# Performance work log

Measured on AMD Instinct MI355X. Metric: run time of the kernel, lower is better.

## Reference

```python
import jax, jax.numpy as jnp
import numpy as np

B, NG, H, G, T0, T1 = 4096, 3000, 6, 30, 500, 50  # batch, genes, hidden, genes/term, leaf terms, mid terms
EPS = 1e-5  # BatchNorm1d default eps


def _bn(x, gamma, beta):
    # training-mode BatchNorm1d: biased batch stats over the batch axis
    m = x.mean(axis=0)
    v = ((x - m) ** 2).mean(axis=0)
    return gamma * (x - m) / jnp.sqrt(v + EPS) + beta


def setup_inputs() -> dict:
    key = jax.random.key(0)
    ks = iter(jax.random.split(key, 32))
    rn = lambda shape, s=0.05: jax.random.normal(next(ks), shape, dtype=jnp.float32) * s
    return dict(
        cell_features=jax.random.normal(next(ks), (B, NG), dtype=jnp.float32),
        Wdg=rn((T0 + T1 + 1, G, NG)), bdg=rn((T0 + T1 + 1, G)),
        W0=rn((T0, H, G)), b0=rn((T0, H)), gam0=jnp.ones((T0, H), jnp.float32), bet0=jnp.zeros((T0, H), jnp.float32),
        aw0=rn((T0, H)), ab0=rn((T0,)), av0=rn((T0,)), ac0=rn((T0,)),
        W1=rn((T1, H, 10 * H + G)), b1=rn((T1, H)), gam1=jnp.ones((T1, H), jnp.float32), bet1=jnp.zeros((T1, H), jnp.float32),
        aw1=rn((T1, H)), ab1=rn((T1,)), av1=rn((T1,)), ac1=rn((T1,)),
        W2=rn((H, T1 * H + G)), b2=rn((H,)), gam2=jnp.ones((H,), jnp.float32), bet2=jnp.zeros((H,), jnp.float32),
        aw2=rn((H,)), ab2=rn(()), av2=rn(()), ac2=rn(()),
    )


def reference(cell_features, Wdg, bdg,
              W0, b0, gam0, bet0, aw0, ab0, av0, ac0,
              W1, b1, gam1, bet1, aw1, ab1, av1, ac1,
              W2, b2, gam2, bet2, aw2, ab2, av2, ac2):
    # direct_gene_layer for every term: Linear(ngene -> genes_per_term), no activation
    dg = jnp.einsum('bn,tgn->btg', cell_features, Wdg) + bdg  # [B, 551, G]
    # ---- layer 0 (leaves): input = direct gene output only ----
    z0 = jnp.tanh(jnp.einsum('btg,thg->bth', dg[:, :T0], W0) + b0)
    n0 = _bn(z0, gam0, bet0)                                   # [B, T0, H]
    aux0 = jnp.tanh(jnp.einsum('bth,th->bt', n0, aw0) + ab0) * av0 + ac0
    # ---- layer 1: term t's children are leaves [10t, 10t+10); concat children + direct genes ----
    in1 = jnp.concatenate([n0.reshape(B, T1, 10 * H), dg[:, T0:T0 + T1]], axis=-1)  # [B, T1, 90]
    z1 = jnp.tanh(jnp.einsum('bti,thi->bth', in1, W1) + b1)
    n1 = _bn(z1, gam1, bet1)                                   # [B, T1, H]
    aux1 = jnp.tanh(jnp.einsum('bth,th->bt', n1, aw1) + ab1) * av1 + ac1
    # ---- root: children = all mid terms + direct genes ----
    in2 = jnp.concatenate([n1.reshape(B, T1 * H), dg[:, -1]], axis=-1)  # [B, 330]
    z2 = jnp.tanh(in2 @ W2.T + b2)
    n2 = _bn(z2, gam2, bet2)                                   # [B, H]
    aux2 = jnp.tanh(n2 @ aw2 + ab2) * av2 + ac2                # [B]
    # flatten (aux_out_map, term_NN_out_map) into one array for a single comparable output
    aux_all = jnp.concatenate([aux0, aux1, aux2[:, None]], axis=1)              # [B, 551]
    nn_all = jnp.concatenate([n0.reshape(B, -1), n1.reshape(B, -1), n2], axis=1)  # [B, 551*H]
    return jnp.concatenate([aux_all, nn_all], axis=1)          # [B, 3857]
```

## Files before the change

kernel.cpp:

```cpp
#include <hip/hip_runtime.h>
#include <hip/hip_bf16.h>

#define BATCH 4096
#define NGENE 3000
#define HID   6
#define GPT   30
#define T0N   500
#define T1N   50
#define KP    3008
#define MROWS 4608
#define OUTW  3857
#define BNEPS 1e-5f

typedef __attribute__((ext_vector_type(8))) __bf16 bf16x8;
typedef __attribute__((ext_vector_type(4))) float f32x4;
typedef __attribute__((ext_vector_type(8))) unsigned short ushort8;

__device__ __forceinline__ unsigned short f2bf(float f) {
  unsigned int u = __builtin_bit_cast(unsigned int, f);
  u = (u + 0x7fffu + ((u >> 16) & 1u)) >> 16;
  return (unsigned short)u;
}

__device__ __forceinline__ void gload_lds16(const void* g, void* l) {
  __builtin_amdgcn_global_load_lds(
      (const __attribute__((address_space(1))) unsigned int*)g,
      (__attribute__((address_space(3))) unsigned int*)l, 16, 0, 0);
}

__global__ void cast_cell(const float* __restrict__ x, ushort8* __restrict__ y) {
  int idx = blockIdx.x * 256 + threadIdx.x;
  int r = idx / 376, c8 = idx - r * 376;
  int c = c8 * 8;
  ushort8 o = (ushort8)0;
  if (c < NGENE) {
    const float4* p = (const float4*)(x + (size_t)r * NGENE + c);
    float4 a = p[0], b = p[1];
    o[0] = f2bf(a.x); o[1] = f2bf(a.y); o[2] = f2bf(a.z); o[3] = f2bf(a.w);
    o[4] = f2bf(b.x); o[5] = f2bf(b.y); o[6] = f2bf(b.z); o[7] = f2bf(b.w);
  }
  y[idx] = o;
}

__global__ void v0_build(const float* __restrict__ Wdg, const float* __restrict__ W0,
                         unsigned short* __restrict__ abuf) {
  int n = blockIdx.x * 256 + threadIdx.x;
  int t = blockIdx.y;
  if (n >= KP) return;
  bool valid = n < NGENE;
  float x[GPT];
#pragma unroll
  for (int g = 0; g < GPT; ++g)
    x[g] = valid ? Wdg[((size_t)(t * GPT + g)) * NGENE + n] : 0.f;
#pragma unroll
  for (int h = 0; h < HID; ++h) {
    const float* w = W0 + (t * HID + h) * GPT;
    float s = 0.f;
#pragma unroll
    for (int g = 0; g < GPT; ++g) s += x[g] * w[g];
    abuf[((size_t)(t * HID + h)) * KP + n] = valid ? f2bf(s) : (unsigned short)0;
  }
}

__global__ void cast_wdg_mid(const float* __restrict__ w, ushort8* __restrict__ y) {
  int idx = blockIdx.x * 256 + threadIdx.x;
  if (idx >= 1530 * 376) return;
  int r = idx / 376, c8 = idx - r * 376;
  int c = c8 * 8;
  ushort8 o = (ushort8)0;
  if (c < NGENE) {
    const float4* p = (const float4*)(w + (size_t)(15000 + r) * NGENE + c);
    float4 a = p[0], b = p[1];
    o[0] = f2bf(a.x); o[1] = f2bf(a.y); o[2] = f2bf(a.z); o[3] = f2bf(a.w);
    o[4] = f2bf(b.x); o[5] = f2bf(b.y); o[6] = f2bf(b.z); o[7] = f2bf(b.w);
  }
  y[(size_t)(3000 + r) * 376 + c8] = o;
}

__global__ void zero_tail(ushort8* __restrict__ y) {
  int idx = blockIdx.x * 256 + threadIdx.x;
  if (idx < 78 * 376) y[(size_t)4530 * 376 + idx] = (ushort8)0;
}

__global__ void build_bias(const float* __restrict__ bdg, const float* __restrict__ W0,
                           const float* __restrict__ b0, float* __restrict__ bias) {
  int idx = blockIdx.x * 256 + threadIdx.x;
  if (idx >= MROWS) return;
  float v = 0.f;
  if (idx < 3000) {
    int t = idx / HID;
    float s = b0[idx];
#pragma unroll
    for (int g = 0; g < GPT; ++g) s += W0[idx * GPT + g] * bdg[t * GPT + g];
    v = s;
  } else if (idx < 4530) {
    v = bdg[15000 + idx - 3000];
  }
  bias[idx] = v;
}

__global__ __launch_bounds__(256) void gemm_fused(
    const unsigned short* __restrict__ A,
    const unsigned short* __restrict__ Bt,
    const float* __restrict__ bias,
    float* __restrict__ C) {
  __shared__ unsigned short smem[8192];
  const int tid  = threadIdx.x;
  const int wave = tid >> 6, lane = tid & 63;
  const int wm = wave >> 1, wn = wave & 1;
  const int quad = lane >> 4, fr = lane & 15;
  const int m0 = blockIdx.y * 128, n0 = blockIdx.x * 128;
  const int lrow = lane >> 2;
  const int lcol = (lane & 3) * 8;

  f32x4 acc[16] = {};

  for (int kt = 0; kt < KP / 32; ++kt) {
    const int k0 = kt * 32;
#pragma unroll
    for (int q = 0; q < 4; ++q) {
      int chunk = q * 4 + wave;
      const unsigned short* gsrc;
      if (chunk < 8) {
        int row = m0 + chunk * 16 + lrow;
        gsrc = A + (size_t)row * KP + k0 + lcol;
      } else {
        int row = n0 + (chunk - 8) * 16 + lrow;
        gsrc = Bt + (size_t)row * KP + k0 + lcol;
      }
      gload_lds16(gsrc, &smem[chunk * 512]);
    }
    asm volatile("s_waitcnt vmcnt(0)" ::: "memory");
    __syncthreads();

    bf16x8 af[4], bfr[4];
#pragma unroll
    for (int tm = 0; tm < 4; ++tm)
      af[tm] = ((const bf16x8*)smem)[((wm * 64 + tm * 16 + fr) * 32 + quad * 8) >> 3];
#pragma unroll
    for (int tn = 0; tn < 4; ++tn)
      bfr[tn] = ((const bf16x8*)smem)[(4096 + (wn * 64 + tn * 16 + fr) * 32 + quad * 8) >> 3];
#pragma unroll
    for (int tm = 0; tm < 4; ++tm)
#pragma unroll
      for (int tn = 0; tn < 4; ++tn)
        acc[tm * 4 + tn] = __builtin_amdgcn_mfma_f32_16x16x32_bf16(
            af[tm], bfr[tn], acc[tm * 4 + tn], 0, 0, 0);
    __syncthreads();
  }

#pragma unroll
  for (int tm = 0; tm < 4; ++tm) {
#pragma unroll
    for (int tn = 0; tn < 4; ++tn) {
      int n = n0 + wn * 64 + tn * 16 + fr;
#pragma unroll
      for (int r = 0; r < 4; ++r) {
        int m = m0 + wm * 64 + tm * 16 + quad * 4 + r;
        float v = acc[tm * 4 + tn][r] + bias[m];
        if (m < 3000) v = tanhf(v);
        C[(size_t)m * BATCH + n] = v;
      }
    }
  }
}

__global__ void colstatsT(const float* __restrict__ zT, float* __restrict__ st, int ncols) {
  int c = blockIdx.x;
  if (c >= ncols) return;
  const float* p = zT + (size_t)c * BATCH;
  float s = 0.f, q = 0.f;
  for (int i = threadIdx.x; i < BATCH; i += 256) {
    float v = p[i];
    s += v; q += v * v;
  }
#pragma unroll
  for (int off = 32; off > 0; off >>= 1) {
    s += __shfl_down(s, off);
    q += __shfl_down(q, off);
  }
  __shared__ float ls[8];
  int lane = threadIdx.x & 63, w = threadIdx.x >> 6;
  if (lane == 0) { ls[2 * w] = s; ls[2 * w + 1] = q; }
  __syncthreads();
  if (threadIdx.x == 0) {
    st[2 * c]     = ls[0] + ls[2] + ls[4] + ls[6];
    st[2 * c + 1] = ls[1] + ls[3] + ls[5] + ls[7];
  }
}

__global__ void bnfin(const float* __restrict__ st, const float* __restrict__ gam,
                      const float* __restrict__ bet, float* __restrict__ ss, int ncols) {
  int c = blockIdx.x * 256 + threadIdx.x;
  if (c >= ncols) return;
  float m = st[2 * c] * (1.f / BATCH);
  float v = st[2 * c + 1] * (1.f / BATCH) - m * m;
  float sc = gam[c] * rsqrtf(v + BNEPS);
  ss[2 * c] = sc;
  ss[2 * c + 1] = bet[c] - m * sc;
}

__global__ void norm_emit(const float* __restrict__ zT, const float* __restrict__ ss,
                          float* __restrict__ out, int ncols, int outoff) {
  __shared__ float tile[64][65];
  int lane = threadIdx.x & 63, w = threadIdx.x >> 6;
  int c0 = blockIdx.x * 64, b0 = blockIdx.y * 64;
#pragma unroll
  for (int i = 0; i < 16; ++i) {
    int cc = w * 16 + i, c = c0 + cc;
    float n = 0.f;
    if (c < ncols)
      n = zT[(size_t)c * BATCH + b0 + lane] * ss[2 * c] + ss[2 * c + 1];
    tile[cc][lane] = n;
  }
  __syncthreads();
  int c = c0 + lane;
  if (c < ncols) {
#pragma unroll
    for (int i = 0; i < 16; ++i) {
      int rr = w * 16 + i;
      out[(size_t)(b0 + rr) * OUTW + outoff + c] = tile[lane][rr];
    }
  }
}

__global__ void aux_head(const float* __restrict__ zT, const float* __restrict__ ss,
                         const float* __restrict__ aw, const float* __restrict__ ab,
                         const float* __restrict__ av, const float* __restrict__ ac,
                         float* __restrict__ out, int nterm, int auxoff) {
  int lane = threadIdx.x & 63, tg = threadIdx.x >> 6;
  int t = blockIdx.x * 4 + tg;
  if (t >= nterm) return;
  int b = blockIdx.y * 64 + lane;
  float s = ab[t];
#pragma unroll
  for (int h = 0; h < HID; ++h) {
    int c = t * HID + h;
    float n = zT[(size_t)c * BATCH + b] * ss[2 * c] + ss[2 * c + 1];
    s += n * aw[c];
  }
  out[(size_t)b * OUTW + auxoff + t] = tanhf(s) * av[t] + ac[t];
}

__global__ void layer1_zT(const float* __restrict__ C, const float* __restrict__ ss0,
                          const float* __restrict__ W1, const float* __restrict__ b1,
                          float* __restrict__ z1T, float* __restrict__ st) {
  int lane = threadIdx.x & 63, tg = threadIdx.x >> 6;
  int t = blockIdx.x * 4 + tg;
  if (t >= T1N) return;
  int b = blockIdx.y * 64 + lane;
  const float* z0T = C;
  const float* dgm = C + (size_t)3000 * BATCH;
  float x[90];
#pragma unroll
  for (int j = 0; j < 60; ++j) {
    int c = t * 60 + j;
    x[j] = z0T[(size_t)c * BATCH + b] * ss0[2 * c] + ss0[2 * c + 1];
  }
#pragma unroll
  for (int g = 0; g < GPT; ++g)
    x[60 + g] = dgm[(size_t)(t * GPT + g) * BATCH + b];
#pragma unroll
  for (int h = 0; h < HID; ++h) {
    int c = t * HID + h;
    const float* w = W1 + c * 90;
    float s = b1[c];
#pragma unroll
    for (int i = 0; i < 90; ++i) s += x[i] * w[i];
    float z = tanhf(s);
    z1T[(size_t)c * BATCH + b] = z;
    float s1 = z, s2 = z * z;
#pragma unroll
    for (int off = 32; off > 0; off >>= 1) {
      s1 += __shfl_down(s1, off);
      s2 += __shfl_down(s2, off);
    }
    if (lane == 0) {
      atomicAdd(&st[2 * c], s1);
      atomicAdd(&st[2 * c + 1], s2);
    }
  }
}

__global__ void root_zT(const float* __restrict__ C, const float* __restrict__ z1T,
                        const float* __restrict__ ss1, const float* __restrict__ W2,
                        const float* __restrict__ b2, float* __restrict__ z2T,
                        float* __restrict__ st) {
  int b = blockIdx.x * 256 + threadIdx.x;
  int lane = threadIdx.x & 63;
  const float* dgr = C + (size_t)4500 * BATCH;
  float s[HID];
#pragma unroll
  for (int h = 0; h < HID; ++h) s[h] = b2[h];
  for (int c = 0; c < 300; ++c) {
    float n = z1T[(size_t)c * BATCH + b] * ss1[2 * c] + ss1[2 * c + 1];
#pragma unroll
    for (int h = 0; h < HID; ++h) s[h] += n * W2[h * 330 + c];
  }
#pragma unroll
  for (int g = 0; g < GPT; ++g) {
    float d = dgr[(size_t)g * BATCH + b];
#pragma unroll
    for (int h = 0; h < HID; ++h) s[h] += d * W2[h * 330 + 300 + g];
  }
#pragma unroll
  for (int h = 0; h < HID; ++h) {
    float z = tanhf(s[h]);
    z2T[(size_t)h * BATCH + b] = z;
    float s1 = z, s2 = z * z;
#pragma unroll
    for (int off = 32; off > 0; off >>= 1) {
      s1 += __shfl_down(s1, off);
      s2 += __shfl_down(s2, off);
    }
    if (lane == 0) {
      atomicAdd(&st[2 * h], s1);
      atomicAdd(&st[2 * h + 1], s2);
    }
  }
}

__global__ void root_emit(const float* __restrict__ z2T, const float* __restrict__ ss2,
                          const float* __restrict__ aw2, const float* __restrict__ ab2,
                          const float* __restrict__ av2, const float* __restrict__ ac2,
                          float* __restrict__ out) {
  int b = blockIdx.x * 256 + threadIdx.x;
  float s = ab2[0];
#pragma unroll
  for (int h = 0; h < HID; ++h) {
    float n = z2T[(size_t)h * BATCH + b] * ss2[2 * h] + ss2[2 * h + 1];
    out[(size_t)b * OUTW + 3851 + h] = n;
    s += n * aw2[h];
  }
  out[(size_t)b * OUTW + 550] = tanhf(s) * av2[0] + ac2[0];
}

extern "C" void kernel_launch(void* const* d_in, const int* in_sizes, int n_in,
                              void* d_out, int out_size, void* d_ws, size_t ws_size,
                              hipStream_t stream) {
  (void)in_sizes; (void)n_in; (void)out_size; (void)ws_size;
  const float* cell = (const float*)d_in[0];
  const float* Wdg  = (const float*)d_in[1];
  const float* bdg  = (const float*)d_in[2];
  const float* W0   = (const float*)d_in[3];
  const float* b0   = (const float*)d_in[4];
  const float* gam0 = (const float*)d_in[5];
  const float* bet0 = (const float*)d_in[6];
  const float* aw0  = (const float*)d_in[7];
  const float* ab0  = (const float*)d_in[8];
  const float* av0  = (const float*)d_in[9];
  const float* ac0  = (const float*)d_in[10];
  const float* W1   = (const float*)d_in[11];
  const float* b1   = (const float*)d_in[12];
  const float* gam1 = (const float*)d_in[13];
  const float* bet1 = (const float*)d_in[14];
  const float* aw1  = (const float*)d_in[15];
  const float* ab1  = (const float*)d_in[16];
  const float* av1  = (const float*)d_in[17];
  const float* ac1  = (const float*)d_in[18];
  const float* W2   = (const float*)d_in[19];
  const float* b2   = (const float*)d_in[20];
  const float* gam2 = (const float*)d_in[21];
  const float* bet2 = (const float*)d_in[22];
  const float* aw2  = (const float*)d_in[23];
  const float* ab2  = (const float*)d_in[24];
  const float* av2  = (const float*)d_in[25];
  const float* ac2  = (const float*)d_in[26];
  float* out = (float*)d_out;

  char* ws = (char*)d_ws;
  unsigned short* cellb = (unsigned short*)(ws);
  unsigned short* abuf  = (unsigned short*)(ws + 24641536);
  float*          C     = (float*)(ws + 52363264);
  float*          z1T   = (float*)(ws + 127860736);
  float*          z2T   = (float*)(ws + 132775936);
  float*          st    = (float*)(ws + 132874240);
  float*          ssb   = (float*)(ws + 132907008);
  float*          bias  = (float*)(ws + 132939776);
  float* st0 = st,  *st1 = st + 2 * 3000,  *st2 = st + 2 * 3300;
  float* ss0 = ssb, *ss1 = ssb + 2 * 3000, *ss2 = ssb + 2 * 3300;

  hipMemsetAsync(st, 0, 32768, stream);
  cast_cell<<<6016, 256, 0, stream>>>(cell, (ushort8*)cellb);
  v0_build<<<dim3(12, T0N), 256, 0, stream>>>(Wdg, W0, abuf);
  cast_wdg_mid<<<2248, 256, 0, stream>>>(Wdg, (ushort8*)abuf);
  zero_tail<<<115, 256, 0, stream>>>((ushort8*)abuf);
  build_bias<<<18, 256, 0, stream>>>(bdg, W0, b0, bias);

  gemm_fused<<<dim3(32, 36), 256, 0, stream>>>(abuf, cellb, bias, C);

  colstatsT<<<3000, 256, 0, stream>>>(C, st0, 3000);
  bnfin<<<12, 256, 0, stream>>>(st0, gam0, bet0, ss0, 3000);
  norm_emit<<<dim3(47, 64), 256, 0, stream>>>(C, ss0, out, 3000, 551);
  aux_head<<<dim3(125, 64), 256, 0, stream>>>(C, ss0, aw0, ab0, av0, ac0, out, 500, 0);

  layer1_zT<<<dim3(13, 64), 256, 0, stream>>>(C, ss0, W1, b1, z1T, st1);
  bnfin<<<2, 256, 0, stream>>>(st1, gam1, bet1, ss1, 300);
  norm_emit<<<dim3(5, 64), 256, 0, stream>>>(z1T, ss1, out, 300, 3551);
  aux_head<<<dim3(13, 64), 256, 0, stream>>>(z1T, ss1, aw1, ab1, av1, ac1, out, 50, 500);

  root_zT<<<16, 256, 0, stream>>>(C, z1T, ss1, W2, b2, z2T, st2);
  bnfin<<<1, 256, 0, stream>>>(st2, gam2, bet2, ss2, 6);
  root_emit<<<16, 256, 0, stream>>>(z2T, ss2, aw2, ab2, av2, ac2, out);
}
```

Before: 693.2 us.

## Rewrite GEMM with triple-buffered swizzled LDS pipeline and fused BN column stats

Replaces the single-buffered 128x128 GEMM with a 256x128-tile, 512-thread kernel. It uses a 3-stage LDS ring of 64-wide K slices with XOR-swizzled layout, interleaved prefetch and MFMA phases, s_setprio, and an XCD-aware block remap. The epilogue now computes per-row sum and sum-of-squares with shuffles and atomics, which removes the separate colstatsT pass over C. It also folds zero_tail into cast_wdg_mid. The atomic accumulation makes the stats nondeterministic, and the large dynamic LDS allocation limits occupancy.

After: 734.9 us. 6.0% more time.

```diff
diff --git a/kernel.cpp b/kernel.cpp
--- a/kernel.cpp
+++ b/kernel.cpp
@@ -11,6 +11,8 @@
 #define MROWS 4608
 #define OUTW  3857
 #define BNEPS 1e-5f
+#define NKT   47
+#define LDSU  24576
 
 typedef __attribute__((ext_vector_type(8))) __bf16 bf16x8;
 typedef __attribute__((ext_vector_type(4))) float f32x4;
@@ -64,22 +66,17 @@
 
 __global__ void cast_wdg_mid(const float* __restrict__ w, ushort8* __restrict__ y) {
   int idx = blockIdx.x * 256 + threadIdx.x;
-  if (idx >= 1530 * 376) return;
+  if (idx >= 1608 * 376) return;
   int r = idx / 376, c8 = idx - r * 376;
   int c = c8 * 8;
   ushort8 o = (ushort8)0;
-  if (c < NGENE) {
+  if (r < 1530 && c < NGENE) {
     const float4* p = (const float4*)(w + (size_t)(15000 + r) * NGENE + c);
     float4 a = p[0], b = p[1];
     o[0] = f2bf(a.x); o[1] = f2bf(a.y); o[2] = f2bf(a.z); o[3] = f2bf(a.w);
     o[4] = f2bf(b.x); o[5] = f2bf(b.y); o[6] = f2bf(b.z); o[7] = f2bf(b.w);
   }
   y[(size_t)(3000 + r) * 376 + c8] = o;
-}
-
-__global__ void zero_tail(ushort8* __restrict__ y) {
-  int idx = blockIdx.x * 256 + threadIdx.x;
-  if (idx < 78 * 376) y[(size_t)4530 * 376 + idx] = (ushort8)0;
 }
 
 __global__ void build_bias(const float* __restrict__ bdg, const float* __restrict__ W0,
@@ -99,93 +96,178 @@
   bias[idx] = v;
 }
 
-__global__ __launch_bounds__(256) void gemm_fused(
+__global__ __launch_bounds__(512, 2) void gemm_fused(
     const unsigned short* __restrict__ A,
     const unsigned short* __restrict__ Bt,
     const float* __restrict__ bias,
-    float* __restrict__ C) {
-  __shared__ unsigned short smem[8192];
+    float* __restrict__ C,
+    float* __restrict__ st) {
+  extern __shared__ unsigned short smem[];
   const int tid  = threadIdx.x;
   const int wave = tid >> 6, lane = tid & 63;
   const int wm = wave >> 1, wn = wave & 1;
-  const int quad = lane >> 4, fr = lane & 15;
-  const int m0 = blockIdx.y * 128, n0 = blockIdx.x * 128;
-  const int lrow = lane >> 2;
-  const int lcol = (lane & 3) * 8;
-
-  f32x4 acc[16] = {};
-
-  for (int kt = 0; kt < KP / 32; ++kt) {
-    const int k0 = kt * 32;
-#pragma unroll
-    for (int q = 0; q < 4; ++q) {
-      int chunk = q * 4 + wave;
-      const unsigned short* gsrc;
-      if (chunk < 8) {
-        int row = m0 + chunk * 16 + lrow;
-        gsrc = A + (size_t)row * KP + k0 + lcol;
-      } else {
-        int row = n0 + (chunk - 8) * 16 + lrow;
-        gsrc = Bt + (size_t)row * KP + k0 + lcol;
+  const int quad = lane >> 4, fr = lane & 15, fs = lane & 7;
+
+  const int bid = blockIdx.x;
+  const int wg  = (bid & 7) * 72 + (bid >> 3);
+  const int m0 = (wg >> 5) * 256;
+  const int n0 = (wg & 31) * 128;
+
+  const int s0 = tid, s1 = tid + 512;
+  const int r0 = s0 >> 3, k0 = s0 & 7;
+  const int r1 = s1 >> 3, k1 = s1 & 7;
+  const unsigned short* gA00 = A  + (size_t)(m0 + r0) * KP + ((k0 ^ (r0 & 7)) << 3);
+  const unsigned short* gA01 = A  + (size_t)(m0 + r1) * KP + ((k1 ^ (r1 & 7)) << 3);
+  const unsigned short* gA10 = gA00 + (size_t)128 * KP;
+  const unsigned short* gA11 = gA01 + (size_t)128 * KP;
+  const unsigned short* gB00 = Bt + (size_t)(n0 + r0) * KP + ((k0 ^ (r0 & 7)) << 3);
+  const unsigned short* gB01 = Bt + (size_t)(n0 + r1) * KP + ((k1 ^ (r1 & 7)) << 3);
+  const int d0 = (wave * 64) * 8;
+  const int d1 = (512 + wave * 64) * 8;
+
+  f32x4 acc[4][4] = {};
+
+#pragma unroll
+  for (int t = 0; t < 2; ++t) {
+    unsigned short* base = smem + t * LDSU;
+    const int ko = t * 64;
+    gload_lds16(gA00 + ko, base + d0);
+    gload_lds16(gA01 + ko, base + d1);
+    gload_lds16(gA10 + ko, base + 8192 + d0);
+    gload_lds16(gA11 + ko, base + 8192 + d1);
+    gload_lds16(gB00 + ko, base + 16384 + d0);
+    gload_lds16(gB01 + ko, base + 16384 + d1);
+  }
+  asm volatile("s_waitcnt vmcnt(6)" ::: "memory");
+  __builtin_amdgcn_s_barrier();
+
+  const int arow0 = (wm * 64 + fr) * 64;
+  const int brow0 = (wn * 64 + fr) * 64;
+  const int ksw0 = ((quad ^ fs) << 3);
+  const int ksw1 = ksw0 ^ 32;
+
+  int cur = 0;
+  for (int t = 0; t < NKT; ++t) {
+    const unsigned short* Ab = smem + cur * LDSU;
+    const unsigned short* Bb = Ab + 16384;
+    int stg = cur + 2; if (stg >= 3) stg -= 3;
+    unsigned short* sb = smem + stg * LDSU;
+    const bool pf = t < NKT - 2;
+    const int ko = (t + 2) * 64;
+
+    bf16x8 a0[2][2], a1[2][2], b0[2][2], b1[2][2];
+#pragma unroll
+    for (int f = 0; f < 2; ++f) {
+      a0[f][0] = *(const bf16x8*)(Ab + arow0 + f * 1024 + ksw0);
+      a0[f][1] = *(const bf16x8*)(Ab + arow0 + f * 1024 + ksw1);
+      b0[f][0] = *(const bf16x8*)(Bb + brow0 + f * 1024 + ksw0);
+      b0[f][1] = *(const bf16x8*)(Bb + brow0 + f * 1024 + ksw1);
+    }
+    if (pf) {
+      gload_lds16(gA00 + ko, sb + d0);
+      gload_lds16(gA01 + ko, sb + d1);
+    }
+    __builtin_amdgcn_s_barrier();
+    asm volatile("s_waitcnt lgkmcnt(0)" ::: "memory");
+    __builtin_amdgcn_s_setprio(1);
+#pragma unroll
+    for (int i = 0; i < 2; ++i)
+#pragma unroll
+      for (int j = 0; j < 2; ++j)
+#pragma unroll
+        for (int k = 0; k < 2; ++k)
+          acc[i][j] = __builtin_amdgcn_mfma_f32_16x16x32_bf16(a0[i][k], b0[j][k], acc[i][j], 0, 0, 0);
+    __builtin_amdgcn_s_setprio(0);
+    __builtin_amdgcn_s_barrier();
+#pragma unroll
+    for (int f = 0; f < 2; ++f) {
+      b1[f][0] = *(const bf16x8*)(Bb + brow0 + (f + 2) * 1024 + ksw0);
+      b1[f][1] = *(const bf16x8*)(Bb + brow0 + (f + 2) * 1024 + ksw1);
+    }
+    if (pf) {
+      gload_lds16(gA10 + ko, sb + 8192 + d0);
+      gload_lds16(gA11 + ko, sb + 8192 + d1);
+    }
+    __builtin_amdgcn_s_barrier();
+    asm volatile("s_waitcnt lgkmcnt(0)" ::: "memory");
+    __builtin_amdgcn_s_setprio(1);
+#pragma unroll
+    for (int i = 0; i < 2; ++i)
+#pragma unroll
+      for (int j = 0; j < 2; ++j)
+#pragma unroll
+        for (int k = 0; k < 2; ++k)
+          acc[i][2 + j] = __builtin_amdgcn_mfma_f32_16x16x32_bf16(a0[i][k], b1[j][k], acc[i][2 + j], 0, 0, 0);
+    __builtin_amdgcn_s_setprio(0);
+    __builtin_amdgcn_s_barrier();
+#pragma unroll
+    for (int f = 0; f < 2; ++f) {
+      a1[f][0] = *(const bf16x8*)(Ab + arow0 + (f + 2) * 1024 + ksw0);
+      a1[f][1] = *(const bf16x8*)(Ab + arow0 + (f + 2) * 1024 + ksw1);
+    }
+    if (pf) {
+      gload_lds16(gB00 + ko, sb + 16384 + d0);
+      gload_lds16(gB01 + ko, sb + 16384 + d1);
+    }
+    __builtin_amdgcn_s_barrier();
+    asm volatile("s_waitcnt lgkmcnt(0)" ::: "memory");
+    __builtin_amdgcn_s_setprio(1);
+#pragma unroll
+    for (int i = 0; i < 2; ++i)
+#pragma unroll
+      for (int j = 0; j < 2; ++j)
+#pragma unroll
+        for (int k = 0; k < 2; ++k)
+          acc[2 + i][2 + j] = __builtin_amdgcn_mfma_f32_16x16x32_bf16(a1[i][k], b1[j][k], acc[2 + i][2 + j], 0, 0, 0);
+    __builtin_amdgcn_s_setprio(0);
+    __builtin_amdgcn_s_barrier();
+    __builtin_amdgcn_s_setprio(1);
+#pragma unroll
+    for (int i = 0; i < 2; ++i)
+#pragma unroll
+      for (int j = 0; j < 2; ++j)
+#pragma unroll
+        for (int k = 0; k < 2; ++k)
+          acc[2 + i][j] = __builtin_amdgcn_mfma_f32_16x16x32_bf16(a1[i][k], b0[j][k], acc[2 + i][j], 0, 0, 0);
+    __builtin_amdgcn_s_setprio(0);
+    if (pf) {
+      asm volatile("s_waitcnt vmcnt(6)" ::: "memory");
+    } else {
+      asm volatile("s_waitcnt vmcnt(0)" ::: "memory");
+    }
+    __builtin_amdgcn_s_barrier();
+    cur += 1; if (cur == 3) cur = 0;
+  }
+
+  const int mbase = m0 + wm * 64 + quad * 4;
+  const int nbase = n0 + wn * 64 + fr;
+#pragma unroll
+  for (int i = 0; i < 4; ++i) {
+#pragma unroll
+    for (int r = 0; r < 4; ++r) {
+      const int m = mbase + i * 16 + r;
+      const float bia = bias[m];
+      const bool act = m < 3000;
+      float s = 0.f, q = 0.f;
+#pragma unroll
+      for (int j = 0; j < 4; ++j) {
+        float v = acc[i][j][r] + bia;
+        if (act) v = tanhf(v);
+        C[(size_t)m * BATCH + nbase + j * 16] = v;
+        s += v; q += v * v;
       }
-      gload_lds16(gsrc, &smem[chunk * 512]);
-    }
-    asm volatile("s_waitcnt vmcnt(0)" ::: "memory");
-    __syncthreads();
-
-    bf16x8 af[4], bfr[4];
-#pragma unroll
-    for (int tm = 0; tm < 4; ++tm)
-      af[tm] = ((const bf16x8*)smem)[((wm * 64 + tm * 16 + fr) * 32 + quad * 8) >> 3];
-#pragma unroll
-    for (int tn = 0; tn < 4; ++tn)
-      bfr[tn] = ((const bf16x8*)smem)[(4096 + (wn * 64 + tn * 16 + fr) * 32 + quad * 8) >> 3];
-#pragma unroll
-    for (int tm = 0; tm < 4; ++tm)
-#pragma unroll
-      for (int tn = 0; tn < 4; ++tn)
-        acc[tm * 4 + tn] = __builtin_amdgcn_mfma_f32_16x16x32_bf16(
-            af[tm], bfr[tn], acc[tm * 4 + tn], 0, 0, 0);
-    __syncthreads();
-  }
-
-#pragma unroll
-  for (int tm = 0; tm < 4; ++tm) {
-#pragma unroll
-    for (int tn = 0; tn < 4; ++tn) {
-      int n = n0 + wn * 64 + tn * 16 + fr;
-#pragma unroll
-      for (int r = 0; r < 4; ++r) {
-        int m = m0 + wm * 64 + tm * 16 + quad * 4 + r;
-        float v = acc[tm * 4 + tn][r] + bias[m];
-        if (m < 3000) v = tanhf(v);
-        C[(size_t)m * BATCH + n] = v;
+      if (act) {
+#pragma unroll
+        for (int off = 1; off < 16; off <<= 1) {
+          s += __shfl_xor(s, off);
+          q += __shfl_xor(q, off);
+        }
+        if (fr == 0) {
+          atomicAdd(&st[2 * m], s);
+          atomicAdd(&st[2 * m + 1], q);
+        }
       }
     }
-  }
-}
-
-__global__ void colstatsT(const float* __restrict__ zT, float* __restrict__ st, int ncols) {
-  int c = blockIdx.x;
-  if (c >= ncols) return;
-  const float* p = zT + (size_t)c * BATCH;
-  float s = 0.f, q = 0.f;
-  for (int i = threadIdx.x; i < BATCH; i += 256) {
-    float v = p[i];
-    s += v; q += v * v;
-  }
-#pragma unroll
-  for (int off = 32; off > 0; off >>= 1) {
-    s += __shfl_down(s, off);
-    q += __shfl_down(q, off);
-  }
-  __shared__ float ls[8];
-  int lane = threadIdx.x & 63, w = threadIdx.x >> 6;
-  if (lane == 0) { ls[2 * w] = s; ls[2 * w + 1] = q; }
-  __syncthreads();
-  if (threadIdx.x == 0) {
-    st[2 * c]     = ls[0] + ls[2] + ls[4] + ls[6];
-    st[2 * c + 1] = ls[1] + ls[3] + ls[5] + ls[7];
   }
 }
 
@@ -380,16 +462,21 @@
   float* st0 = st,  *st1 = st + 2 * 3000,  *st2 = st + 2 * 3300;
   float* ss0 = ssb, *ss1 = ssb + 2 * 3000, *ss2 = ssb + 2 * 3300;
 
+  static int s_attr = 0;
+  if (!s_attr) {
+    hipFuncSetAttribute(reinterpret_cast<const void*>(gemm_fused),
+                        hipFuncAttributeMaxDynamicSharedMemorySize, 147456);
+    s_attr = 1;
+  }
+
   hipMemsetAsync(st, 0, 32768, stream);
   cast_cell<<<6016, 256, 0, stream>>>(cell, (ushort8*)cellb);
   v0_build<<<dim3(12, T0N), 256, 0, stream>>>(Wdg, W0, abuf);
-  cast_wdg_mid<<<2248, 256, 0, stream>>>(Wdg, (ushort8*)abuf);
-  zero_tail<<<115, 256, 0, stream>>>((ushort8*)abuf);
+  cast_wdg_mid<<<2362, 256, 0, stream>>>(Wdg, (ushort8*)abuf);
   build_bias<<<18, 256, 0, stream>>>(bdg, W0, b0, bias);
 
-  gemm_fused<<<dim3(32, 36), 256, 0, stream>>>(abuf, cellb, bias, C);
-
-  colstatsT<<<3000, 256, 0, stream>>>(C, st0, 3000);
+  gemm_fused<<<576, 512, 147456, stream>>>(abuf, cellb, bias, C, st0);
+
   bnfin<<<12, 256, 0, stream>>>(st0, gam0, bet0, ss0, 3000);
   norm_emit<<<dim3(47, 64), 256, 0, stream>>>(C, ss0, out, 3000, 551);
   aux_head<<<dim3(125, 64), 256, 0, stream>>>(C, ss0, aw0, ab0, av0, ac0, out, 500, 0);
```
